# Kernel optimization log

Measured on AMD Instinct MI355X. Metric: run time of the kernel, lower is better.

The kernel has to match this reference:

```python
import jax, jax.numpy as jnp
import numpy as np

NEG = -1e30
H = 768

def mask_logits(target, mask):
    return target * mask + (1.0 - mask) * NEG

def setup_inputs() -> dict:
    key = jax.random.key(0)
    ks = jax.random.split(key, 8)
    B, CL, QL = 16, 512, 64
    c = jax.random.normal(ks[0], (B, CL, H), dtype=jnp.float32)
    q = jax.random.normal(ks[1], (B, QL, H), dtype=jnp.float32)
    c_mask = jnp.ones((B, CL), dtype=jnp.float32)
    q_mask = jnp.ones((B, QL), dtype=jnp.float32)
    # nn.Linear(768,1) weights (kaiming-ish scale) and biases
    std = 1.0 / np.sqrt(H)
    w_c = jax.random.normal(ks[2], (H,), dtype=jnp.float32) * std
    w_q = jax.random.normal(ks[3], (H,), dtype=jnp.float32) * std
    w_cq = jax.random.normal(ks[4], (H,), dtype=jnp.float32) * std
    b_c = jax.random.normal(ks[5], (), dtype=jnp.float32) * std
    b_q = jax.random.normal(ks[6], (), dtype=jnp.float32) * std
    b_cq = jax.random.normal(ks[7], (), dtype=jnp.float32) * std
    return {"c": c, "q": q, "c_mask": c_mask, "q_mask": q_mask,
            "w_c": w_c, "b_c": b_c, "w_q": w_q, "b_q": b_q,
            "w_cq": w_cq, "b_cq": b_cq}

def reference(c, q, c_mask, q_mask, w_c, b_c, w_q, b_q, w_cq, b_cq):
    # c: (B, c_len, H), q: (B, q_len, H)
    cm = c_mask[:, :, None]   # (B, c_len, 1)
    qm = q_mask[:, None, :]   # (B, 1, q_len)
    # per-query loop in torch == trilinear term: ((c*w_cq) @ q^T) + b_cq
    cq = jnp.einsum('bid,bjd->bij', c * w_cq, q) + b_cq      # (B, c_len, q_len)
    s = (c @ w_c + b_c)[:, :, None] + (q @ w_q + b_q)[:, None, :] + cq
    a = jax.nn.softmax(mask_logits(s, qm), axis=2)            # (B, c_len, q_len)
    c2q = jnp.einsum('bij,bjd->bid', a, q)                    # (B, c_len, H)
    b_att = jax.nn.softmax(jnp.max(mask_logits(s, cm), axis=2), axis=1)  # (B, c_len)
    q2c = jnp.einsum('bi,bid->bd', b_att, c)[:, None, :]      # (B, 1, H)
    x = jnp.concatenate([c, c2q, c * c2q, c * q2c], axis=-1)  # (B, c_len, 4H)
    return x
```

## Files before the change

kernel.cpp:

```cpp
#include <hip/hip_runtime.h>
#include <math.h>
#include <stdint.h>

#define NEGV -1e30f
typedef unsigned short u16;
typedef unsigned int u32;
typedef short bfx8 __attribute__((ext_vector_type(8)));
typedef float f32x4 __attribute__((ext_vector_type(4)));

constexpr int B_  = 16;
constexpr int CL  = 512;
constexpr int QL  = 64;
constexpr int H   = 768;
constexpr int OD  = 4 * H;
constexpr int IT  = 16;

constexpr size_t WS_QW     = 0;
constexpr size_t WS_ROWMAX = 1024;
constexpr size_t WS_PART   = 17408;
constexpr size_t WS_QBF    = 422912;
constexpr size_t WS_QTF    = 816128;

__device__ __forceinline__ u16 f2b(float x) {
  u32 u = __float_as_uint(x);
  u += 0x7FFFu + ((u >> 16) & 1u);
  return (u16)(u >> 16);
}
__device__ __forceinline__ float wredmax(float v) {
#pragma unroll
  for (int off = 32; off; off >>= 1) v = fmaxf(v, __shfl_xor(v, off));
  return v;
}
__device__ __forceinline__ float wredsum(float v) {
#pragma unroll
  for (int off = 32; off; off >>= 1) v += __shfl_xor(v, off);
  return v;
}

__global__ __launch_bounds__(256) void k_qprep(const float* __restrict__ q,
                                               const float* __restrict__ w_cq,
                                               const float* __restrict__ w_q,
                                               const float* __restrict__ b_q,
                                               const float* __restrict__ b_cq,
                                               u16* __restrict__ qbF,
                                               u16* __restrict__ qTF,
                                               float* __restrict__ qw) {
  const int ch = blockIdx.x, bb = blockIdx.y, t = threadIdx.x;
  if (ch == 6) {
    int j = t >> 2, qt = t & 3;
    const float* qr = q + ((size_t)bb * QL + j) * H;
    float s = 0.f;
#pragma unroll 8
    for (int p = 0; p < 48; ++p) {
      float4 v = *(const float4*)(qr + (qt * 48 + p) * 4);
      float4 w = *(const float4*)(w_q + (qt * 48 + p) * 4);
      s += v.x * w.x + v.y * w.y + v.z * w.z + v.w * w.w;
    }
    s += __shfl_xor(s, 1);
    s += __shfl_xor(s, 2);
    if (qt == 0) qw[bb * QL + j] = s + b_q[0] + b_cq[0];
    return;
  }
  __shared__ u16 tR[64 * 132], tS[64 * 132];
  const int d0 = ch * 128;
#pragma unroll
  for (int s2 = 0; s2 < 8; ++s2) {
    int idx = t + s2 * 256, j = idx >> 5, d4 = idx & 31;
    size_t go = ((size_t)(bb * QL + j)) * H + d0 + d4 * 4;
    float4 v = *(const float4*)(q + go);
    float4 w = *(const float4*)(w_cq + d0 + d4 * 4);
    uint2 raw, scl;
    raw.x = f2b(v.x) | ((u32)f2b(v.y) << 16);
    raw.y = f2b(v.z) | ((u32)f2b(v.w) << 16);
    scl.x = f2b(v.x * w.x) | ((u32)f2b(v.y * w.y) << 16);
    scl.y = f2b(v.z * w.z) | ((u32)f2b(v.w * w.w) << 16);
    *(uint2*)&tR[j * 132 + d4 * 4] = raw;
    *(uint2*)&tS[j * 132 + d4 * 4] = scl;
  }
  __syncthreads();
  {
    int l = t & 63, jt = t >> 6, lr = l & 15, lg = l >> 4;
#pragma unroll
    for (int kt = 0; kt < 4; ++kt) {
      u16 vals[8];
#pragma unroll
      for (int e = 0; e < 8; ++e)
        vals[e] = tS[(jt * 16 + lr) * 132 + kt * 32 + lg * 8 + e];
      uint4 pk;
      pk.x = vals[0] | ((u32)vals[1] << 16);
      pk.y = vals[2] | ((u32)vals[3] << 16);
      pk.z = vals[4] | ((u32)vals[5] << 16);
      pk.w = vals[6] | ((u32)vals[7] << 16);
      *(uint4*)(qbF + ((((size_t)bb * 4 + jt) * 24) + ch * 4 + kt) * 512 + l * 8) = pk;
    }
  }
  {
#pragma unroll
    for (int rep = 0; rep < 4; ++rep) {
      int idx = rep * 256 + t;
      int l = idx & 63, h = (idx >> 6) & 1, uul = idx >> 7;
      int lr = l & 15, lg = l >> 4;
      u16 vals[8];
#pragma unroll
      for (int e = 0; e < 8; ++e)
        vals[e] = tR[(h * 32 + lg * 8 + e) * 132 + uul * 16 + lr];
      uint4 pk;
      pk.x = vals[0] | ((u32)vals[1] << 16);
      pk.y = vals[2] | ((u32)vals[3] << 16);
      pk.z = vals[4] | ((u32)vals[5] << 16);
      pk.w = vals[6] | ((u32)vals[7] << 16);
      *(uint4*)(qTF + (((size_t)bb * 48 + ch * 8 + uul) * 2 + h) * 512 + l * 8) = pk;
    }
  }
}

__global__ __launch_bounds__(256, 4) void ka(const float* __restrict__ c,
                                             const float* __restrict__ c_mask,
                                             const float* __restrict__ q_mask,
                                             const float* __restrict__ w_c,
                                             const float* __restrict__ b_c,
                                             const float* __restrict__ qw,
                                             const u16* __restrict__ qbF,
                                             const u16* __restrict__ qTF,
                                             float* __restrict__ rowmax,
                                             float* __restrict__ out) {
  __shared__ __align__(16) u16 cA[IT * H];
  __shared__ float sS[IT * 68];
  __shared__ u16 aS[IT * 64];

  const int t = threadIdx.x, lane = t & 63;
  const int wid = __builtin_amdgcn_readfirstlane(t >> 6);
  const int bb = blockIdx.y, i0 = blockIdx.x * IT;
  const int lr = lane & 15, lg = lane >> 4;
  const int sw = (lr & 7) << 4;

  const u16* qbp = qbF + (((size_t)bb * 4 + wid) * 24) * 512 + lane * 8;
  const u16* qtp = qTF + (size_t)bb * 49152 + lane * 8;

  bfx8 qpf0 = *(const bfx8*)(qbp);
  bfx8 qpf1 = *(const bfx8*)(qbp + 512);

  float cwq = 0.f;
  {
    int row = t >> 4, c4b = t & 15;
    size_t cb0 = ((size_t)bb * CL + i0 + row) * H;
#pragma unroll
    for (int u = 0; u < 12; ++u) {
      int col4 = c4b + u * 16;
      float4 v = *(const float4*)(c + cb0 + col4 * 4);
      float4 w = *(const float4*)(w_c + col4 * 4);
      cwq += v.x * w.x + v.y * w.y + v.z * w.z + v.w * w.w;
      uint2 pk;
      pk.x = f2b(v.x) | ((u32)f2b(v.y) << 16);
      pk.y = f2b(v.z) | ((u32)f2b(v.w) << 16);
      int byte = row * 1536 + ((col4 * 8) ^ ((row & 7) << 4));
      *(uint2*)((char*)cA + byte) = pk;
    }
    cwq += __shfl_xor(cwq, 1);
    cwq += __shfl_xor(cwq, 2);
    cwq += __shfl_xor(cwq, 4);
    cwq += __shfl_xor(cwq, 8);
  }
  const float qw_r = qw[bb * QL + lane];
  const float qm_r = q_mask[bb * QL + lane];
  const float bc = b_c[0];
  __syncthreads();

  f32x4 acc0 = {0.f, 0.f, 0.f, 0.f}, acc1 = {0.f, 0.f, 0.f, 0.f};
  {
    const char* ap = (const char*)cA + lr * 1536;
    acc0 = __builtin_amdgcn_mfma_f32_16x16x32_bf16(
        *(const bfx8*)(ap + ((lg * 16) ^ sw)), qpf0, acc0, 0, 0, 0);
    acc1 = __builtin_amdgcn_mfma_f32_16x16x32_bf16(
        *(const bfx8*)(ap + ((64 + lg * 16) ^ sw)), qpf1, acc1, 0, 0, 0);
#pragma unroll
    for (int kt = 2; kt < 24; kt += 2) {
      bfx8 av0 = *(const bfx8*)(ap + ((kt * 64 + lg * 16) ^ sw));
      bfx8 av1 = *(const bfx8*)(ap + (((kt + 1) * 64 + lg * 16) ^ sw));
      bfx8 bv0 = *(const bfx8*)(qbp + kt * 512);
      bfx8 bv1 = *(const bfx8*)(qbp + (kt + 1) * 512);
      acc0 = __builtin_amdgcn_mfma_f32_16x16x32_bf16(av0, bv0, acc0, 0, 0, 0);
      acc1 = __builtin_amdgcn_mfma_f32_16x16x32_bf16(av1, bv1, acc1, 0, 0, 0);
    }
  }
  bfx8 pf0 = *(const bfx8*)(qtp + (size_t)(wid * 12 + 0) * 1024);
  bfx8 pf1 = *(const bfx8*)(qtp + (size_t)(wid * 12 + 0) * 1024 + 512);
  bfx8 pf2 = *(const bfx8*)(qtp + (size_t)(wid * 12 + 1) * 1024);
  bfx8 pf3 = *(const bfx8*)(qtp + (size_t)(wid * 12 + 1) * 1024 + 512);
#pragma unroll
  for (int m = 0; m < 4; ++m)
    sS[(lg * 4 + m) * 68 + wid * 16 + lr] = acc0[m] + acc1[m];
  __syncthreads();

#pragma unroll
  for (int rr = 0; rr < 4; ++rr) {
    int r = wid * 4 + rr;
    float s = sS[r * 68 + lane] + qw_r;
    float mraw = wredmax(s);
    float sm = (qm_r > 0.5f) ? s : NEGV;
    float mm = wredmax(sm);
    float p = __expf(sm - mm);
    float ps = wredsum(p);
    float a = p / ps;
    float cwr = __shfl(cwq, rr * 16);
    if (lane == 0) {
      float cmv = c_mask[bb * CL + i0 + r];
      rowmax[bb * CL + i0 + r] = (cmv > 0.5f) ? (mraw + cwr + bc) : NEGV;
    }
    int byte = r * 128 + ((lane * 2) ^ ((r & 7) << 4));
    *(u16*)((char*)aS + byte) = f2b(a);
  }
  __syncthreads();

  bfx8 a0 = *(const bfx8*)((char*)aS + lr * 128 + ((lg * 16) ^ sw));
  bfx8 a1 = *(const bfx8*)((char*)aS + lr * 128 + ((64 + lg * 16) ^ sw));
  f32x4 o[12];
  {
    f32x4 v0 = {0.f, 0.f, 0.f, 0.f};
    v0 = __builtin_amdgcn_mfma_f32_16x16x32_bf16(pf0, a0, v0, 0, 0, 0);
    v0 = __builtin_amdgcn_mfma_f32_16x16x32_bf16(pf1, a1, v0, 0, 0, 0);
    o[0] = v0;
    f32x4 v1 = {0.f, 0.f, 0.f, 0.f};
    v1 = __builtin_amdgcn_mfma_f32_16x16x32_bf16(pf2, a0, v1, 0, 0, 0);
    v1 = __builtin_amdgcn_mfma_f32_16x16x32_bf16(pf3, a1, v1, 0, 0, 0);
    o[1] = v1;
  }
#pragma unroll
  for (int u = 2; u < 12; ++u) {
    int uu = wid * 12 + u;
    bfx8 b0 = *(const bfx8*)(qtp + (size_t)uu * 1024);
    bfx8 b1 = *(const bfx8*)(qtp + (size_t)uu * 1024 + 512);
    f32x4 v = {0.f, 0.f, 0.f, 0.f};
    v = __builtin_amdgcn_mfma_f32_16x16x32_bf16(b0, a0, v, 0, 0, 0);
    v = __builtin_amdgcn_mfma_f32_16x16x32_bf16(b1, a1, v, 0, 0, 0);
    o[u] = v;
  }

  {
    size_t grow = (size_t)bb * CL + i0 + lr;
    const float* crow = c + grow * H;
    float* ob = out + grow * OD;
#pragma unroll
    for (int u = 0; u < 12; ++u) {
      int d4 = (wid * 12 + u) * 16 + lg * 4;
      float4 cv = *(const float4*)(crow + d4);
      float4 ov = make_float4(o[u][0], o[u][1], o[u][2], o[u][3]);
      *(float4*)(ob + d4) = cv;
      *(float4*)(ob + H + d4) = ov;
      *(float4*)(ob + 2 * H + d4) = make_float4(cv.x * ov.x, cv.y * ov.y,
                                                cv.z * ov.z, cv.w * ov.w);
    }
  }
}

__global__ __launch_bounds__(256) void kb(const float* __restrict__ rowmax,
                                          const float* __restrict__ c,
                                          float* __restrict__ part) {
  int s = blockIdx.x, b = blockIdx.y, t = threadIdx.x;
  __shared__ float red[8];
  __shared__ float ba[32];
  float v0 = rowmax[b * CL + t], v1 = rowmax[b * CL + t + 256];
  float m = wredmax(fmaxf(v0, v1));
  if ((t & 63) == 0) red[t >> 6] = m;
  __syncthreads();
  m = fmaxf(fmaxf(red[0], red[1]), fmaxf(red[2], red[3]));
  float p = __expf(v0 - m) + __expf(v1 - m);
  p = wredsum(p);
  if ((t & 63) == 0) red[4 + (t >> 6)] = p;
  __syncthreads();
  float ssum = red[4] + red[5] + red[6] + red[7];
  if (t < 32) ba[t] = __expf(rowmax[b * CL + s * 32 + t] - m) / ssum;
  __syncthreads();
  if (t < 192) {
    const float* cb = c + ((size_t)b * CL + s * 32) * H;
    float4 acc = make_float4(0.f, 0.f, 0.f, 0.f);
#pragma unroll 8
    for (int r = 0; r < 32; ++r) {
      float w = ba[r];
      float4 cv = *(const float4*)(cb + (size_t)r * H + t * 4);
      acc.x += w * cv.x; acc.y += w * cv.y; acc.z += w * cv.z; acc.w += w * cv.w;
    }
    *(float4*)(part + ((size_t)b * 16 + s) * H + t * 4) = acc;
  }
}

__global__ __launch_bounds__(256) void kc2(const float* __restrict__ part,
                                           const float* __restrict__ c,
                                           float* __restrict__ out) {
  __shared__ float4 redS[8][32];
  __shared__ float4 q2cS[32];
  const int b = blockIdx.y;
  const int s = blockIdx.x >> 4, rg = blockIdx.x & 15;
  const int t = threadIdx.x;
  const int grp = t >> 5, col4 = t & 31;
  float4 acc = make_float4(0.f, 0.f, 0.f, 0.f);
#pragma unroll
  for (int u = 0; u < 2; ++u) {
    float4 v = *(const float4*)(part + ((size_t)b * 16 + grp * 2 + u) * H +
                                s * 128 + col4 * 4);
    acc.x += v.x; acc.y += v.y; acc.z += v.z; acc.w += v.w;
  }
  redS[grp][col4] = acc;
  __syncthreads();
  if (t < 32) {
    float4 sum = redS[0][t];
#pragma unroll
    for (int g = 1; g < 8; ++g) {
      float4 v = redS[g][t];
      sum.x += v.x; sum.y += v.y; sum.z += v.z; sum.w += v.w;
    }
    q2cS[t] = sum;
  }
  __syncthreads();
  float4 gv = q2cS[col4];
  const int sub = t >> 5;
#pragma unroll
  for (int r2 = 0; r2 < 4; ++r2) {
    int row = rg * 32 + sub * 4 + r2;
    size_t grow = (size_t)b * CL + row;
    float4 cv = *(const float4*)(c + grow * H + s * 128 + col4 * 4);
    *(float4*)(out + grow * OD + 3 * H + s * 128 + col4 * 4) =
        make_float4(cv.x * gv.x, cv.y * gv.y, cv.z * gv.z, cv.w * gv.w);
  }
}

extern "C" void kernel_launch(void* const* d_in, const int* in_sizes, int n_in,
                              void* d_out, int out_size, void* d_ws, size_t ws_size,
                              hipStream_t stream) {
  const float* c      = (const float*)d_in[0];
  const float* q      = (const float*)d_in[1];
  const float* c_mask = (const float*)d_in[2];
  const float* q_mask = (const float*)d_in[3];
  const float* w_c    = (const float*)d_in[4];
  const float* b_c    = (const float*)d_in[5];
  const float* w_q    = (const float*)d_in[6];
  const float* b_q    = (const float*)d_in[7];
  const float* w_cq   = (const float*)d_in[8];
  const float* b_cq   = (const float*)d_in[9];
  float* out = (float*)d_out;
  float* ws  = (float*)d_ws;
  float* qw     = ws + WS_QW;
  float* rowmax = ws + WS_ROWMAX;
  float* part   = ws + WS_PART;
  u16*   qbF    = (u16*)(ws + WS_QBF);
  u16*   qTF    = (u16*)(ws + WS_QTF);

  k_qprep<<<dim3(7, B_), 256, 0, stream>>>(q, w_cq, w_q, b_q, b_cq, qbF, qTF, qw);
  ka<<<dim3(CL / IT, B_), 256, 0, stream>>>(c, c_mask, q_mask, w_c, b_c,
                                            qw, qbF, qTF, rowmax, out);
  kb<<<dim3(16, B_), 256, 0, stream>>>(rowmax, c, part);
  kc2<<<dim3(96, B_), 256, 0, stream>>>(part, c, out);
}
```

Measured before the change: 58.38 us.

## Fuse q2c reduction and broadcast-multiply into one column-sliced kernel

Merges the two q2c kernels into one. Each block now owns a 64-column slice of one batch across all 512 rows, so it can reduce the weighted sum locally and then write c*q2c without a partial buffer or an extra launch. This drops the workspace round-trip and one launch. In exchange it cuts the grid to 192 blocks, each walking 512 rows serially twice, which lowers parallelism; the second read of c may hit cache.

Result: slower. 62.12 us (+6.4%).

```diff
diff --git a/kernel.cpp b/kernel.cpp
--- a/kernel.cpp
+++ b/kernel.cpp
@@ -17,7 +17,6 @@
 
 constexpr size_t WS_QW     = 0;
 constexpr size_t WS_ROWMAX = 1024;
-constexpr size_t WS_PART   = 17408;
 constexpr size_t WS_QBF    = 422912;
 constexpr size_t WS_QTF    = 816128;
 
@@ -253,73 +252,57 @@
   }
 }
 
-__global__ __launch_bounds__(256) void kb(const float* __restrict__ rowmax,
+__global__ __launch_bounds__(256) void kq(const float* __restrict__ rowmax,
                                           const float* __restrict__ c,
-                                          float* __restrict__ part) {
-  int s = blockIdx.x, b = blockIdx.y, t = threadIdx.x;
+                                          float* __restrict__ out) {
   __shared__ float red[8];
-  __shared__ float ba[32];
+  __shared__ float baS[CL];
+  __shared__ float4 redS[16][17];
+  __shared__ float4 q2cS[16];
+  const int b = blockIdx.y, s = blockIdx.x, t = threadIdx.x;
+
   float v0 = rowmax[b * CL + t], v1 = rowmax[b * CL + t + 256];
   float m = wredmax(fmaxf(v0, v1));
   if ((t & 63) == 0) red[t >> 6] = m;
   __syncthreads();
   m = fmaxf(fmaxf(red[0], red[1]), fmaxf(red[2], red[3]));
-  float p = __expf(v0 - m) + __expf(v1 - m);
-  p = wredsum(p);
-  if ((t & 63) == 0) red[4 + (t >> 6)] = p;
-  __syncthreads();
-  float ssum = red[4] + red[5] + red[6] + red[7];
-  if (t < 32) ba[t] = __expf(rowmax[b * CL + s * 32 + t] - m) / ssum;
-  __syncthreads();
-  if (t < 192) {
-    const float* cb = c + ((size_t)b * CL + s * 32) * H;
-    float4 acc = make_float4(0.f, 0.f, 0.f, 0.f);
+  float p0 = __expf(v0 - m), p1 = __expf(v1 - m);
+  float ps = wredsum(p0 + p1);
+  if ((t & 63) == 0) red[4 + (t >> 6)] = ps;
+  __syncthreads();
+  float inv = 1.0f / (red[4] + red[5] + red[6] + red[7]);
+  baS[t] = p0 * inv;
+  baS[t + 256] = p1 * inv;
+  __syncthreads();
+
+  const int rg = t >> 4, c4 = t & 15;
+  const float* cb = c + (size_t)b * CL * H + s * 64 + c4 * 4;
+  float4 acc = make_float4(0.f, 0.f, 0.f, 0.f);
 #pragma unroll 8
-    for (int r = 0; r < 32; ++r) {
-      float w = ba[r];
-      float4 cv = *(const float4*)(cb + (size_t)r * H + t * 4);
-      acc.x += w * cv.x; acc.y += w * cv.y; acc.z += w * cv.z; acc.w += w * cv.w;
-    }
-    *(float4*)(part + ((size_t)b * 16 + s) * H + t * 4) = acc;
-  }
-}
-
-__global__ __launch_bounds__(256) void kc2(const float* __restrict__ part,
-                                           const float* __restrict__ c,
-                                           float* __restrict__ out) {
-  __shared__ float4 redS[8][32];
-  __shared__ float4 q2cS[32];
-  const int b = blockIdx.y;
-  const int s = blockIdx.x >> 4, rg = blockIdx.x & 15;
-  const int t = threadIdx.x;
-  const int grp = t >> 5, col4 = t & 31;
-  float4 acc = make_float4(0.f, 0.f, 0.f, 0.f);
-#pragma unroll
-  for (int u = 0; u < 2; ++u) {
-    float4 v = *(const float4*)(part + ((size_t)b * 16 + grp * 2 + u) * H +
-                                s * 128 + col4 * 4);
-    acc.x += v.x; acc.y += v.y; acc.z += v.z; acc.w += v.w;
-  }
-  redS[grp][col4] = acc;
-  __syncthreads();
-  if (t < 32) {
+  for (int r = rg; r < CL; r += 16) {
+    float w = baS[r];
+    float4 cv = *(const float4*)(cb + (size_t)r * H);
+    acc.x += w * cv.x; acc.y += w * cv.y; acc.z += w * cv.z; acc.w += w * cv.w;
+  }
+  redS[rg][c4] = acc;
+  __syncthreads();
+  if (t < 16) {
     float4 sum = redS[0][t];
 #pragma unroll
-    for (int g = 1; g < 8; ++g) {
+    for (int g = 1; g < 16; ++g) {
       float4 v = redS[g][t];
       sum.x += v.x; sum.y += v.y; sum.z += v.z; sum.w += v.w;
     }
     q2cS[t] = sum;
   }
   __syncthreads();
-  float4 gv = q2cS[col4];
-  const int sub = t >> 5;
-#pragma unroll
-  for (int r2 = 0; r2 < 4; ++r2) {
-    int row = rg * 32 + sub * 4 + r2;
-    size_t grow = (size_t)b * CL + row;
-    float4 cv = *(const float4*)(c + grow * H + s * 128 + col4 * 4);
-    *(float4*)(out + grow * OD + 3 * H + s * 128 + col4 * 4) =
+  const float4 gv = q2cS[c4];
+
+  float* ob = out + (size_t)b * CL * OD + 3 * H + s * 64 + c4 * 4;
+#pragma unroll 8
+  for (int r = rg; r < CL; r += 16) {
+    float4 cv = *(const float4*)(cb + (size_t)r * H);
+    *(float4*)(ob + (size_t)r * OD) =
         make_float4(cv.x * gv.x, cv.y * gv.y, cv.z * gv.z, cv.w * gv.w);
   }
 }
@@ -341,13 +324,11 @@
   float* ws  = (float*)d_ws;
   float* qw     = ws + WS_QW;
   float* rowmax = ws + WS_ROWMAX;
-  float* part   = ws + WS_PART;
   u16*   qbF    = (u16*)(ws + WS_QBF);
   u16*   qTF    = (u16*)(ws + WS_QTF);
 
   k_qprep<<<dim3(7, B_), 256, 0, stream>>>(q, w_cq, w_q, b_q, b_cq, qbF, qTF, qw);
   ka<<<dim3(CL / IT, B_), 256, 0, stream>>>(c, c_mask, q_mask, w_c, b_c,
                                             qw, qbF, qTF, rowmax, out);
-  kb<<<dim3(16, B_), 256, 0, stream>>>(rowmax, c, part);
-  kc2<<<dim3(96, B_), 256, 0, stream>>>(part, c, out);
-}
+  kq<<<dim3(12, B_), 256, 0, stream>>>(rowmax, c, out);
+}
```
